# Optimization experiments

Hardware: AMD Instinct MI355X
Metric: run time of the kernel (lower is better)

The kernel has to match this reference:

```python
import jax, jax.numpy as jnp
import numpy as np

N_FULL, N_LOCAL, N_GLOBAL = 6, 4, 2
N_HEADS = N_FULL + N_LOCAL + N_GLOBAL
WINDOW = 64
DIM = 1536
B, S = 2, 2048


def setup_inputs() -> dict:
    key = jax.random.key(0)
    k0, k1, k2 = jax.random.split(key, 3)
    sc = DIM ** -0.5
    return {
        "x": jax.random.normal(k0, (B, S, DIM), dtype=jnp.float32),
        "Wqkv": jax.random.normal(k1, (DIM, 3 * DIM), dtype=jnp.float32) * sc,
        "bqkv": jnp.zeros((3 * DIM,), dtype=jnp.float32),
        "Wout": jax.random.normal(k2, (DIM, DIM), dtype=jnp.float32) * sc,
        "bout": jnp.zeros((DIM,), dtype=jnp.float32),
    }


def _attend(q, k, v, scale, bias=None):
    # q,k,v: [B,H,S,D]
    scores = jnp.einsum("bhqd,bhkd->bhqk", q, k) * scale
    if bias is not None:
        scores = scores + bias
    p = jax.nn.softmax(scores, axis=-1)
    return jnp.einsum("bhqk,bhkd->bhqd", p, v)


def reference(x, Wqkv, bqkv, Wout, bout):
    Bb, Ss, D = x.shape
    hd = D // N_HEADS
    scale = hd ** -0.5
    qkv = (x @ Wqkv + bqkv).reshape(Bb, Ss, 3, N_HEADS, hd)
    qkv = jnp.transpose(qkv, (2, 0, 3, 1, 4))  # [3,B,H,S,hd]
    q, k, v = qkv[0], qkv[1], qkv[2]
    h1 = N_FULL
    h2 = N_FULL + N_LOCAL

    # tier 1: full attention on first n_full heads
    out_full = _attend(q[:, :h1], k[:, :h1], v[:, :h1], scale)

    # tier 2: sliding-window (|i-j| <= window//2 allowed) on next n_local heads
    idx = jnp.arange(Ss)
    allowed = jnp.abs(idx[:, None] - idx[None, :]) <= WINDOW // 2  # [S,S]
    bias = jnp.where(allowed, 0.0, -jnp.inf).astype(x.dtype)[None, None]
    out_local = _attend(q[:, h1:h2], k[:, h1:h2], v[:, h1:h2], scale, bias)

    # tier 3: global — attend only to first and last tokens
    kg = jnp.stack([k[:, h2:, 0], k[:, h2:, -1]], axis=2)  # [B,Hg,2,hd]
    vg = jnp.stack([v[:, h2:, 0], v[:, h2:, -1]], axis=2)
    out_global = _attend(q[:, h2:], kg, vg, scale)

    out = jnp.concatenate([out_full, out_local, out_global], axis=1)  # [B,H,S,hd]
    out = jnp.transpose(out, (0, 2, 1, 3)).reshape(Bb, Ss, D)
    return out @ Wout + bout
```

## Files before the change

kernel.cpp:

```cpp
#include <hip/hip_runtime.h>
#include <hip/hip_bf16.h>

#define SEQ    2048
#define TOK    4096
#define DMODEL 1536
#define QKVROW 4608
#define HD     128
#define SCALE  0.08838834764831845f

#define NSPLIT 4
#define KRANGE (SEQ / NSPLIT)
#define NPAIR  12
#define ROWS_P (NPAIR * SEQ)
#define OPART_ELEMS ((size_t)ROWS_P * HD)

typedef __attribute__((ext_vector_type(8))) short short8;
typedef __attribute__((ext_vector_type(4))) short short4v;
typedef __attribute__((ext_vector_type(4))) float f32x4;

__device__ __forceinline__ float b2f(short s) {
    union { unsigned u; float f; } x;
    x.u = ((unsigned)(unsigned short)s) << 16;
    return x.f;
}
__device__ __forceinline__ short f2b(float f) {
    union { float f; unsigned u; } x; x.f = f;
    unsigned u = x.u;
    unsigned r = (u + 0x7fffu + ((u >> 16) & 1u)) >> 16;
    return (short)r;
}

__device__ __forceinline__ void gld_lds16(const short* g, short* l) {
    __builtin_amdgcn_global_load_lds(
        (__attribute__((address_space(1))) void*)(g),
        (__attribute__((address_space(3))) void*)(l), 16, 0, 0);
}

#define CVT_BLOCKS  6144
#define TQKV_BLOCKS 1728
#define TOUT_BLOCKS 576

__device__ __forceinline__ void transpose_tile(
    const float* __restrict__ W, short* __restrict__ WT,
    int K, int N, int k0, int n0, int t, short (*tile)[65])
{
    {
        int j  = t & 63;
        int i0 = (t >> 6) * 16;
        for (int ii = 0; ii < 16; ++ii)
            tile[i0 + ii][j] = f2b(W[(size_t)(k0 + i0 + ii) * N + n0 + j]);
    }
    __syncthreads();
    {
        int i  = t & 63;
        int j0 = (t >> 6) * 16;
        for (int jj = 0; jj < 16; ++jj)
            WT[(size_t)(n0 + j0 + jj) * K + k0 + i] = tile[i][j0 + jj];
    }
}

__global__ __launch_bounds__(256) void prepass_k(
    const float* __restrict__ x, const float* __restrict__ Wqkv,
    const float* __restrict__ Wout, short* __restrict__ xb,
    short* __restrict__ WqkvT, short* __restrict__ WoutT)
{
    __shared__ short tile[64][65];
    const int bid = blockIdx.x;
    const int t   = threadIdx.x;
    if (bid < CVT_BLOCKS) {
        int i = bid * 1024 + t * 4;
        float4 v = *(const float4*)(x + i);
        short4v b = { f2b(v.x), f2b(v.y), f2b(v.z), f2b(v.w) };
        *(short4v*)(xb + i) = b;
    } else if (bid < CVT_BLOCKS + TQKV_BLOCKS) {
        int tb = bid - CVT_BLOCKS;
        transpose_tile(Wqkv, WqkvT, DMODEL, QKVROW,
                       (tb / (QKVROW / 64)) * 64, (tb % (QKVROW / 64)) * 64, t, tile);
    } else {
        int tb = bid - (CVT_BLOCKS + TQKV_BLOCKS);
        transpose_tile(Wout, WoutT, DMODEL, DMODEL,
                       (tb / (DMODEL / 64)) * 64, (tb % (DMODEL / 64)) * 64, t, tile);
    }
}

template <bool OUT_BF16>
__global__ __launch_bounds__(256) void gemm_tn_k(
    const short* __restrict__ A, const short* __restrict__ BT,
    const float* __restrict__ bias, void* __restrict__ Cout,
    int M, int N, int K)
{
    __shared__ short As[128 * 32];
    __shared__ short Bs[128 * 32];

    const int t    = threadIdx.x;
    const int wave = t >> 6;
    const int lane = t & 63;
    const int quad = lane >> 4;
    const int lo   = lane & 15;
    const int m0   = blockIdx.y * 128;
    const int n0   = blockIdx.x * 128;
    const int wm   = (wave >> 1) * 64;
    const int wn   = (wave & 1) * 64;

    const int srow = wave * 16 + (lane >> 2);
    const int scol = (lane & 3) * 8;

    const short* aP0 = A  + (size_t)(m0 + srow) * K + scol;
    const short* aP1 = A  + (size_t)(m0 + 64 + srow) * K + scol;
    const short* bP0 = BT + (size_t)(n0 + srow) * K + scol;
    const short* bP1 = BT + (size_t)(n0 + 64 + srow) * K + scol;
    short* asD0 = As + (wave * 16) * 32;
    short* asD1 = As + (64 + wave * 16) * 32;
    short* bsD0 = Bs + (wave * 16) * 32;
    short* bsD1 = Bs + (64 + wave * 16) * 32;

    f32x4 acc[4][4];
    for (int i = 0; i < 4; ++i)
        for (int j = 0; j < 4; ++j)
            acc[i][j] = (f32x4){0.f, 0.f, 0.f, 0.f};

    for (int kt = 0; kt < K; kt += 32) {
        gld_lds16(aP0 + kt, asD0);
        gld_lds16(aP1 + kt, asD1);
        gld_lds16(bP0 + kt, bsD0);
        gld_lds16(bP1 + kt, bsD1);
        __syncthreads();

        short8 af[4], bfv[4];
        for (int i = 0; i < 4; ++i) {
            af[i]  = *(const short8*)(As + (wm + i * 16 + lo) * 32 + quad * 8);
            bfv[i] = *(const short8*)(Bs + (wn + i * 16 + lo) * 32 + quad * 8);
        }
        for (int mi = 0; mi < 4; ++mi)
            for (int ni = 0; ni < 4; ++ni)
                acc[mi][ni] = __builtin_amdgcn_mfma_f32_16x16x32_bf16(
                    af[mi], bfv[ni], acc[mi][ni], 0, 0, 0);
        __syncthreads();
    }

    for (int ni = 0; ni < 4; ++ni) {
        int col  = n0 + wn + ni * 16 + lo;
        float bv = bias[col];
        for (int mi = 0; mi < 4; ++mi)
            for (int r = 0; r < 4; ++r) {
                int row = m0 + wm + mi * 16 + quad * 4 + r;
                float val = acc[mi][ni][r] + bv;
                if (OUT_BF16)
                    ((short*)Cout)[(size_t)row * N + col] = f2b(val);
                else
                    ((float*)Cout)[(size_t)row * N + col] = val;
            }
    }
}

#define KSP 136
#define VTP 44
#define PLP 40

__global__ __launch_bounds__(256) void attn_full_split(
    const short* __restrict__ qkv, short* __restrict__ Opart,
    float* __restrict__ lsum)
{
    const int pair = blockIdx.y;
    const int b    = pair / 6;
    const int h    = pair % 6;
    const int q0   = blockIdx.x * 64;
    const int kz   = blockIdx.z;
    const int t    = threadIdx.x;
    const int wave = t >> 6;
    const int lane = t & 63;
    const int quad = lane >> 4;
    const int lo   = lane & 15;

    __shared__ short Ks[32 * KSP];
    __shared__ short Vr[32 * KSP];
    __shared__ short Vt[128 * VTP];
    __shared__ short Pl[4][16 * PLP];

    const short* base = qkv + (size_t)b * SEQ * QKVROW;

    short8 qf[4];
    {
        int qrow = q0 + wave * 16 + lo;
        const short* qp = base + (size_t)qrow * QKVROW + h * HD;
        for (int c = 0; c < 4; ++c)
            qf[c] = *(const short8*)(qp + c * 32 + quad * 8);
    }

    f32x4 o[8];
    for (int i = 0; i < 8; ++i) o[i] = (f32x4){0.f, 0.f, 0.f, 0.f};
    float lrow[4] = {0.f, 0.f, 0.f, 0.f};

    const int skey = t >> 3;
    const int sdc  = (t & 7) * 16;
    const int thd  = t & 127;
    const int tkc  = (t >> 7) * 16;

    const int kend = kz * KRANGE + KRANGE;
    for (int k0 = kz * KRANGE; k0 < kend; k0 += 32) {
        {
            const short* kro = base + (size_t)(k0 + skey) * QKVROW + DMODEL     + h * HD + sdc;
            const short* vro = base + (size_t)(k0 + skey) * QKVROW + 2 * DMODEL + h * HD + sdc;
            short8 ka = *(const short8*)kro;
            short8 kb = *(const short8*)(kro + 8);
            short8 va = *(const short8*)vro;
            short8 vb = *(const short8*)(vro + 8);
            *(short8*)(Ks + skey * KSP + sdc)     = ka;
            *(short8*)(Ks + skey * KSP + sdc + 8) = kb;
            *(short8*)(Vr + skey * KSP + sdc)     = va;
            *(short8*)(Vr + skey * KSP + sdc + 8) = vb;
        }
        __syncthreads();

        {
            short8 x0, x1;
            for (int j = 0; j < 8; ++j) x0[j] = Vr[(tkc + j) * KSP + thd];
            for (int j = 0; j < 8; ++j) x1[j] = Vr[(tkc + 8 + j) * KSP + thd];
            *(short8*)(Vt + thd * VTP + tkc)     = x0;
            *(short8*)(Vt + thd * VTP + tkc + 8) = x1;
        }

        f32x4 s[2];
        s[0] = (f32x4){0.f, 0.f, 0.f, 0.f};
        s[1] = (f32x4){0.f, 0.f, 0.f, 0.f};
        for (int g = 0; g < 2; ++g)
            for (int c = 0; c < 4; ++c) {
                short8 kf = *(const short8*)(Ks + (g * 16 + lo) * KSP + c * 32 + quad * 8);
                s[g] = __builtin_amdgcn_mfma_f32_16x16x32_bf16(qf[c], kf, s[g], 0, 0, 0);
            }

        for (int g = 0; g < 2; ++g)
            for (int r = 0; r < 4; ++r) {
                float p = __expf(s[g][r] * SCALE);
                lrow[r] += p;
                Pl[wave][(quad * 4 + r) * PLP + g * 16 + lo] = f2b(p);
            }
        __syncthreads();

        short8 pf = *(const short8*)(&Pl[wave][lo * PLP + quad * 8]);
        for (int ni = 0; ni < 8; ++ni) {
            short8 vf = *(const short8*)(Vt + (ni * 16 + lo) * VTP + quad * 8);
            o[ni] = __builtin_amdgcn_mfma_f32_16x16x32_bf16(pf, vf, o[ni], 0, 0, 0);
        }
    }

    for (int r = 0; r < 4; ++r)
        for (int off = 1; off < 16; off <<= 1)
            lrow[r] += __shfl_xor(lrow[r], off, 64);

    for (int ni = 0; ni < 8; ++ni)
        for (int r = 0; r < 4; ++r) {
            int grow = pair * SEQ + q0 + wave * 16 + quad * 4 + r;
            Opart[(size_t)kz * OPART_ELEMS + (size_t)grow * HD + ni * 16 + lo] =
                f2b(o[ni][r]);
        }
    if (lo == 0)
        for (int r = 0; r < 4; ++r) {
            int grow = pair * SEQ + q0 + wave * 16 + quad * 4 + r;
            lsum[kz * ROWS_P + grow] = lrow[r];
        }
}

__global__ __launch_bounds__(256) void attn_local_mfma(
    const short* __restrict__ qkv, short* __restrict__ att)
{
    const int pair = blockIdx.y;
    const int b    = pair >> 2;
    const int h    = 6 + (pair & 3);
    const int q0   = blockIdx.x * 64;
    const int t    = threadIdx.x;
    const int wave = t >> 6;
    const int lane = t & 63;
    const int quad = lane >> 4;
    const int lo   = lane & 15;

    __shared__ short Ks[32 * KSP];
    __shared__ short Vr[32 * KSP];
    __shared__ short Vt[128 * VTP];
    __shared__ short Pl[4][16 * PLP];

    const short* base = qkv + (size_t)b * SEQ * QKVROW;

    short8 qf[4];
    {
        int qrow = q0 + wave * 16 + lo;
        const short* qp = base + (size_t)qrow * QKVROW + h * HD;
        for (int c = 0; c < 4; ++c)
            qf[c] = *(const short8*)(qp + c * 32 + quad * 8);
    }

    f32x4 o[8];
    for (int i = 0; i < 8; ++i) o[i] = (f32x4){0.f, 0.f, 0.f, 0.f};
    float lrow[4] = {0.f, 0.f, 0.f, 0.f};

    const int skey = t >> 3;
    const int sdc  = (t & 7) * 16;
    const int thd  = t & 127;
    const int tkc  = (t >> 7) * 16;
    const int irow = q0 + wave * 16 + quad * 4;

    const int ks = max(0, q0 - 32);
    const int ke = min(SEQ, q0 + 96);
    for (int k0 = ks; k0 < ke; k0 += 32) {
        {
            const short* kro = base + (size_t)(k0 + skey) * QKVROW + DMODEL     + h * HD + sdc;
            const short* vro = base + (size_t)(k0 + skey) * QKVROW + 2 * DMODEL + h * HD + sdc;
            short8 ka = *(const short8*)kro;
            short8 kb = *(const short8*)(kro + 8);
            short8 va = *(const short8*)vro;
            short8 vb = *(const short8*)(vro + 8);
            *(short8*)(Ks + skey * KSP + sdc)     = ka;
            *(short8*)(Ks + skey * KSP + sdc + 8) = kb;
            *(short8*)(Vr + skey * KSP + sdc)     = va;
            *(short8*)(Vr + skey * KSP + sdc + 8) = vb;
        }
        __syncthreads();

        {
            short8 x0, x1;
            for (int j = 0; j < 8; ++j) x0[j] = Vr[(tkc + j) * KSP + thd];
            for (int j = 0; j < 8; ++j) x1[j] = Vr[(tkc + 8 + j) * KSP + thd];
            *(short8*)(Vt + thd * VTP + tkc)     = x0;
            *(short8*)(Vt + thd * VTP + tkc + 8) = x1;
        }

        f32x4 s[2];
        s[0] = (f32x4){0.f, 0.f, 0.f, 0.f};
        s[1] = (f32x4){0.f, 0.f, 0.f, 0.f};
        for (int g = 0; g < 2; ++g)
            for (int c = 0; c < 4; ++c) {
                short8 kf = *(const short8*)(Ks + (g * 16 + lo) * KSP + c * 32 + quad * 8);
                s[g] = __builtin_amdgcn_mfma_f32_16x16x32_bf16(qf[c], kf, s[g], 0, 0, 0);
            }

        for (int g = 0; g < 2; ++g)
            for (int r = 0; r < 4; ++r) {
                int j = k0 + g * 16 + lo;
                int d = irow + r - j;
                float p = (d >= -32 && d <= 32) ? __expf(s[g][r] * SCALE) : 0.f;
                lrow[r] += p;
                Pl[wave][(quad * 4 + r) * PLP + g * 16 + lo] = f2b(p);
            }
        __syncthreads();

        short8 pf = *(const short8*)(&Pl[wave][lo * PLP + quad * 8]);
        for (int ni = 0; ni < 8; ++ni) {
            short8 vf = *(const short8*)(Vt + (ni * 16 + lo) * VTP + quad * 8);
            o[ni] = __builtin_amdgcn_mfma_f32_16x16x32_bf16(pf, vf, o[ni], 0, 0, 0);
        }
    }

    for (int r = 0; r < 4; ++r)
        for (int off = 1; off < 16; off <<= 1)
            lrow[r] += __shfl_xor(lrow[r], off, 64);

    for (int ni = 0; ni < 8; ++ni)
        for (int r = 0; r < 4; ++r) {
            int row = irow + r;
            size_t off = ((size_t)(b * SEQ + row)) * DMODEL + h * HD + ni * 16 + lo;
            att[off] = f2b(o[ni][r] / lrow[r]);
        }
}

#define MERGE_BLOCKS  12288
#define GLOBAL_BLOCKS 2048

__global__ __launch_bounds__(256) void postattn_k(
    const short* __restrict__ qkv, const short* __restrict__ Opart,
    const float* __restrict__ lsum, short* __restrict__ att)
{
    const int bid  = blockIdx.x;
    const int t    = threadIdx.x;
    const int wave = t >> 6;
    const int lane = t & 63;

    if (bid < MERGE_BLOCKS) {
        int idx  = bid * 256 + t;
        int pair = idx >> 18;
        int q    = (idx >> 7) & (SEQ - 1);
        int hd   = idx & (HD - 1);
        int row  = pair * SEQ + q;
        float osum = 0.f, ls = 0.f;
        for (int z = 0; z < NSPLIT; ++z) {
            ls   += lsum[z * ROWS_P + row];
            osum += b2f(Opart[(size_t)z * OPART_ELEMS + (size_t)row * HD + hd]);
        }
        int b = pair / 6, h = pair % 6;
        att[((size_t)(b * SEQ + q)) * DMODEL + h * HD + hd] = f2b(osum / ls);
    } else {
        int gb   = bid - MERGE_BLOCKS;
        int pair = gb >> 9;
        int q    = (gb & 511) * 4 + wave;
        int b    = pair >> 1;
        int h    = 10 + (pair & 1);

        const short* base = qkv + (size_t)b * SEQ * QKVROW;
        const short* qp   = base + (size_t)q * QKVROW + h * HD;
        const short* k0   = base + DMODEL + h * HD;
        const short* k1   = base + (size_t)(SEQ - 1) * QKVROW + DMODEL + h * HD;

        float s0 = fmaf(b2f(qp[lane]), b2f(k0[lane]),
                   b2f(qp[lane + 64]) * b2f(k0[lane + 64]));
        float s1 = fmaf(b2f(qp[lane]), b2f(k1[lane]),
                   b2f(qp[lane + 64]) * b2f(k1[lane + 64]));
        for (int off = 1; off < 64; off <<= 1) {
            s0 += __shfl_xor(s0, off, 64);
            s1 += __shfl_xor(s1, off, 64);
        }
        s0 *= SCALE; s1 *= SCALE;
        float m  = fmaxf(s0, s1);
        float e0 = __expf(s0 - m), e1 = __expf(s1 - m);
        float inv = 1.f / (e0 + e1);
        float p0 = e0 * inv, p1 = e1 * inv;

        const short* v0 = base + 2 * DMODEL + h * HD;
        const short* v1 = base + (size_t)(SEQ - 1) * QKVROW + 2 * DMODEL + h * HD;
        size_t ob = ((size_t)(b * SEQ + q)) * DMODEL + h * HD;
        att[ob + lane]      = f2b(fmaf(p0, b2f(v0[lane]),      p1 * b2f(v1[lane])));
        att[ob + lane + 64] = f2b(fmaf(p0, b2f(v0[lane + 64]), p1 * b2f(v1[lane + 64])));
    }
}

extern "C" void kernel_launch(void* const* d_in, const int* in_sizes, int n_in,
                              void* d_out, int out_size, void* d_ws, size_t ws_size,
                              hipStream_t stream) {
    const float* x    = (const float*)d_in[0];
    const float* Wqkv = (const float*)d_in[1];
    const float* bqkv = (const float*)d_in[2];
    const float* Wout = (const float*)d_in[3];
    const float* bout = (const float*)d_in[4];

    char* p = (char*)d_ws;
    short* qkv   = (short*)p;  p += (size_t)TOK * QKVROW * 2;
    short* Opart = (short*)p;  p += OPART_ELEMS * NSPLIT * 2;
    float* lsum  = (float*)p;  p += (size_t)ROWS_P * NSPLIT * 4;
    short* xb    = (short*)p;  p += (size_t)TOK * DMODEL * 2;
    short* att   = xb;
    short* WqkvT = (short*)p;  p += (size_t)QKVROW * DMODEL * 2;
    short* WoutT = (short*)p;

    prepass_k<<<dim3(CVT_BLOCKS + TQKV_BLOCKS + TOUT_BLOCKS), 256, 0, stream>>>(
        x, Wqkv, Wout, xb, WqkvT, WoutT);
    gemm_tn_k<true><<<dim3(QKVROW / 128, TOK / 128), 256, 0, stream>>>(
        xb, WqkvT, bqkv, (void*)qkv, TOK, QKVROW, DMODEL);
    attn_full_split<<<dim3(SEQ / 64, NPAIR, NSPLIT), 256, 0, stream>>>(qkv, Opart, lsum);
    attn_local_mfma<<<dim3(SEQ / 64, 8), 256, 0, stream>>>(qkv, att);
    postattn_k<<<dim3(MERGE_BLOCKS + GLOBAL_BLOCKS), 256, 0, stream>>>(
        qkv, Opart, lsum, att);
    gemm_tn_k<false><<<dim3(DMODEL / 128, TOK / 128), 256, 0, stream>>>(
        att, WoutT, bout, d_out, TOK, DMODEL, DMODEL);
}
```

Measured before the change: 312.8 us.

## Replace GEMM with 256x256-tile 8-wave kernel using double-buffered 8-phase LDS pipeline

Result: slower. 345.8 us (+10.5%).

```diff
diff --git a/kernel.cpp b/kernel.cpp
--- a/kernel.cpp
+++ b/kernel.cpp
@@ -83,68 +83,129 @@
     }
 }
 
+__device__ __forceinline__ short* ldsP(short* base, int slot, int mat, int kh, int st) {
+    return base + (((slot * 2 + mat) * 2 + kh) * 16 + st) * 512;
+}
+
+template <int SLOT, int KH, int G>
+__device__ __forceinline__ void ld_a(short8 af[4], short* smem, int wm8, int lane) {
+#pragma unroll
+    for (int mi = 0; mi < 4; ++mi)
+        af[mi] = *(const short8*)(ldsP(smem, SLOT, 0, KH, wm8 + G * 4 + mi) + lane * 8);
+}
+template <int SLOT, int KH>
+__device__ __forceinline__ void ld_b(short8 bf[4], short* smem, int wn4, int lane) {
+#pragma unroll
+    for (int ni = 0; ni < 4; ++ni)
+        bf[ni] = *(const short8*)(ldsP(smem, SLOT, 1, KH, wn4 + ni) + lane * 8);
+}
+template <int G>
+__device__ __forceinline__ void mfma16(f32x4 (&acc)[8][4], const short8 af[4], const short8 bf[4]) {
+#pragma unroll
+    for (int mi = 0; mi < 4; ++mi)
+#pragma unroll
+        for (int ni = 0; ni < 4; ++ni)
+            acc[G * 4 + mi][ni] = __builtin_amdgcn_mfma_f32_16x16x32_bf16(
+                af[mi], bf[ni], acc[G * 4 + mi][ni], 0, 0, 0);
+}
+
+__device__ __forceinline__ void stage2(const short* g0, const short* g1, int ko,
+                                       short* d0, short* d1) {
+    gld_lds16(g0 + ko, d0);
+    gld_lds16(g1 + ko, d1);
+}
+
+#define STG_A(S, KH, KT) stage2(gA0, gA1, (KT) * 64 + (KH) * 32, \
+        ldsP(smem, (S), 0, (KH), wave), ldsP(smem, (S), 0, (KH), 8 + wave))
+#define STG_B(S, KH, KT) stage2(gB0, gB1, (KT) * 64 + (KH) * 32, \
+        ldsP(smem, (S), 1, (KH), wave), ldsP(smem, (S), 1, (KH), 8 + wave))
+
+#define PH(S, KH, G, LOADB, STG_STMT, VMW)                          \
+    do {                                                            \
+        ld_a<S, KH, G>(af, smem, wm8, lane);                        \
+        if (LOADB) ld_b<S, KH>(bf, smem, wn4, lane);                \
+        STG_STMT;                                                   \
+        asm volatile("" ::: "memory");                              \
+        __builtin_amdgcn_s_barrier();                               \
+        asm volatile("s_waitcnt lgkmcnt(0)" ::: "memory");          \
+        __builtin_amdgcn_s_setprio(1);                              \
+        mfma16<G>(acc, af, bf);                                     \
+        __builtin_amdgcn_s_setprio(0);                              \
+        if (VMW) asm volatile("s_waitcnt vmcnt(6)" ::: "memory");   \
+        asm volatile("" ::: "memory");                              \
+        __builtin_amdgcn_s_barrier();                               \
+        asm volatile("" ::: "memory");                              \
+    } while (0)
+
 template <bool OUT_BF16>
-__global__ __launch_bounds__(256) void gemm_tn_k(
+__global__ __launch_bounds__(512, 2) void gemm256_8ph(
     const short* __restrict__ A, const short* __restrict__ BT,
     const float* __restrict__ bias, void* __restrict__ Cout,
-    int M, int N, int K)
+    int N, int K)
 {
-    __shared__ short As[128 * 32];
-    __shared__ short Bs[128 * 32];
+    __shared__ short smem[2 * 2 * 2 * 16 * 512];
 
     const int t    = threadIdx.x;
     const int wave = t >> 6;
     const int lane = t & 63;
     const int quad = lane >> 4;
     const int lo   = lane & 15;
-    const int m0   = blockIdx.y * 128;
-    const int n0   = blockIdx.x * 128;
-    const int wm   = (wave >> 1) * 64;
-    const int wn   = (wave & 1) * 64;
-
-    const int srow = wave * 16 + (lane >> 2);
-    const int scol = (lane & 3) * 8;
-
-    const short* aP0 = A  + (size_t)(m0 + srow) * K + scol;
-    const short* aP1 = A  + (size_t)(m0 + 64 + srow) * K + scol;
-    const short* bP0 = BT + (size_t)(n0 + srow) * K + scol;
-    const short* bP1 = BT + (size_t)(n0 + 64 + srow) * K + scol;
-    short* asD0 = As + (wave * 16) * 32;
-    short* asD1 = As + (64 + wave * 16) * 32;
-    short* bsD0 = Bs + (wave * 16) * 32;
-    short* bsD1 = Bs + (64 + wave * 16) * 32;
-
-    f32x4 acc[4][4];
-    for (int i = 0; i < 4; ++i)
+    const int wm   = wave >> 2;
+    const int wn   = wave & 3;
+    const int wm8  = wm * 8;
+    const int wn4  = wn * 4;
+    const int bn0  = blockIdx.x * 256;
+    const int bm0  = blockIdx.y * 256;
+
+    const int rO = quad * 8;
+    const short* gA0 = A  + (size_t)(bm0 + wave * 16 + lo) * K + rO;
+    const short* gA1 = A  + (size_t)(bm0 + (8 + wave) * 16 + lo) * K + rO;
+    const short* gB0 = BT + (size_t)(bn0 + wave * 16 + lo) * K + rO;
+    const short* gB1 = BT + (size_t)(bn0 + (8 + wave) * 16 + lo) * K + rO;
+
+    f32x4 acc[8][4];
+#pragma unroll
+    for (int i = 0; i < 8; ++i)
+#pragma unroll
         for (int j = 0; j < 4; ++j)
             acc[i][j] = (f32x4){0.f, 0.f, 0.f, 0.f};
 
-    for (int kt = 0; kt < K; kt += 32) {
-        gld_lds16(aP0 + kt, asD0);
-        gld_lds16(aP1 + kt, asD1);
-        gld_lds16(bP0 + kt, bsD0);
-        gld_lds16(bP1 + kt, bsD1);
-        __syncthreads();
-
-        short8 af[4], bfv[4];
-        for (int i = 0; i < 4; ++i) {
-            af[i]  = *(const short8*)(As + (wm + i * 16 + lo) * 32 + quad * 8);
-            bfv[i] = *(const short8*)(Bs + (wn + i * 16 + lo) * 32 + quad * 8);
-        }
-        for (int mi = 0; mi < 4; ++mi)
-            for (int ni = 0; ni < 4; ++ni)
-                acc[mi][ni] = __builtin_amdgcn_mfma_f32_16x16x32_bf16(
-                    af[mi], bfv[ni], acc[mi][ni], 0, 0, 0);
-        __syncthreads();
-    }
-
+    const int NT = K >> 6;
+
+    STG_A(0, 0, 0); STG_A(0, 1, 0); STG_B(0, 0, 0); STG_B(0, 1, 0);
+    STG_B(1, 0, 1); STG_A(1, 0, 1); STG_B(1, 1, 1);
+    asm volatile("s_waitcnt vmcnt(6)" ::: "memory");
+    asm volatile("" ::: "memory");
+    __builtin_amdgcn_s_barrier();
+    asm volatile("" ::: "memory");
+
+    short8 af[4], bf[4];
+#pragma unroll 1
+    for (int it = 0; it < (NT >> 1); ++it) {
+        const int T  = it * 2;
+        const int t2 = min(T + 2, NT - 1);
+        const int t3 = min(T + 3, NT - 1);
+        PH(0, 0, 0, true,  STG_A(1, 1, T + 1), 0);
+        PH(0, 0, 1, false, STG_B(0, 0, t2),    0);
+        PH(0, 1, 0, true,  STG_A(0, 0, t2),    0);
+        PH(0, 1, 1, false, STG_B(0, 1, t2),    1);
+        PH(1, 0, 0, true,  STG_A(0, 1, t2),    0);
+        PH(1, 0, 1, false, STG_B(1, 0, t3),    0);
+        PH(1, 1, 0, true,  STG_A(1, 0, t3),    0);
+        PH(1, 1, 1, false, STG_B(1, 1, t3),    1);
+    }
+    asm volatile("s_waitcnt vmcnt(0)" ::: "memory");
+
+#pragma unroll
     for (int ni = 0; ni < 4; ++ni) {
-        int col  = n0 + wn + ni * 16 + lo;
+        int col  = bn0 + wn * 64 + ni * 16 + lo;
         float bv = bias[col];
-        for (int mi = 0; mi < 4; ++mi)
+#pragma unroll
+        for (int r8 = 0; r8 < 8; ++r8)
+#pragma unroll
             for (int r = 0; r < 4; ++r) {
-                int row = m0 + wm + mi * 16 + quad * 4 + r;
-                float val = acc[mi][ni][r] + bv;
+                int row   = bm0 + wm * 128 + r8 * 16 + quad * 4 + r;
+                float val = acc[r8][ni][r] + bv;
                 if (OUT_BF16)
                     ((short*)Cout)[(size_t)row * N + col] = f2b(val);
                 else
@@ -441,12 +502,12 @@
 
     prepass_k<<<dim3(CVT_BLOCKS + TQKV_BLOCKS + TOUT_BLOCKS), 256, 0, stream>>>(
         x, Wqkv, Wout, xb, WqkvT, WoutT);
-    gemm_tn_k<true><<<dim3(QKVROW / 128, TOK / 128), 256, 0, stream>>>(
-        xb, WqkvT, bqkv, (void*)qkv, TOK, QKVROW, DMODEL);
+    gemm256_8ph<true><<<dim3(QKVROW / 256, TOK / 256), 512, 0, stream>>>(
+        xb, WqkvT, bqkv, (void*)qkv, QKVROW, DMODEL);
     attn_full_split<<<dim3(SEQ / 64, NPAIR, NSPLIT), 256, 0, stream>>>(qkv, Opart, lsum);
     attn_local_mfma<<<dim3(SEQ / 64, 8), 256, 0, stream>>>(qkv, att);
     postattn_k<<<dim3(MERGE_BLOCKS + GLOBAL_BLOCKS), 256, 0, stream>>>(
         qkv, Opart, lsum, att);
-    gemm_tn_k<false><<<dim3(DMODEL / 128, TOK / 128), 256, 0, stream>>>(
-        att, WoutT, bout, d_out, TOK, DMODEL, DMODEL);
-}
+    gemm256_8ph<false><<<dim3(DMODEL / 256, TOK / 256), 512, 0, stream>>>(
+        att, WoutT, bout, d_out, DMODEL, DMODEL);
+}
```

## Pre-transpose V globally and double-buffer K/V tiles in full attention

Applied to the files above, without the earlier changes.

New measurement: 294.1 us. -6.0%, faster.

```diff
diff --git a/kernel.cpp b/kernel.cpp
--- a/kernel.cpp
+++ b/kernel.cpp
@@ -153,112 +153,153 @@
     }
 }
 
+#define VT_BLOCKS 768
+
+__global__ __launch_bounds__(256) void vtrans_k(
+    const short* __restrict__ qkv, short* __restrict__ vT)
+{
+    __shared__ short tile[64][65];
+    const int bid = blockIdx.x;
+    const int t   = threadIdx.x;
+    const int bh  = bid >> 6;
+    const int rem = bid & 63;
+    const int st  = rem & 31, dt = rem >> 5;
+    const int b   = bh / 6, h = bh % 6;
+    const int s0  = st * 64, d0 = dt * 64;
+
+    const short* src = qkv + (size_t)(b * SEQ + s0) * QKVROW + 2 * DMODEL + h * HD + d0;
+    {
+        int j = t & 63, i0 = (t >> 6) * 16;
+        for (int ii = 0; ii < 16; ++ii)
+            tile[i0 + ii][j] = src[(size_t)(i0 + ii) * QKVROW + j];
+    }
+    __syncthreads();
+    {
+        int i = t & 63, j0 = (t >> 6) * 16;
+        short* dst = vT + ((size_t)(b * 6 + h) * HD + d0) * SEQ + s0;
+        for (int jj = 0; jj < 16; ++jj)
+            dst[(size_t)(j0 + jj) * SEQ + i] = tile[i][j0 + jj];
+    }
+}
+
 #define KSP 136
 #define VTP 44
 #define PLP 40
 
-__global__ __launch_bounds__(256) void attn_full_split(
-    const short* __restrict__ qkv, short* __restrict__ Opart,
-    float* __restrict__ lsum)
+__global__ __launch_bounds__(256, 3) void attn_full_v2(
+    const short* __restrict__ qkv, const short* __restrict__ vT,
+    short* __restrict__ Opart, float* __restrict__ lsum)
 {
     const int pair = blockIdx.y;
     const int b    = pair / 6;
     const int h    = pair % 6;
-    const int q0   = blockIdx.x * 64;
+    const int q0   = blockIdx.x * 128;
     const int kz   = blockIdx.z;
     const int t    = threadIdx.x;
-    const int wave = t >> 6;
+    const int w    = t >> 6;
     const int lane = t & 63;
     const int quad = lane >> 4;
     const int lo   = lane & 15;
 
-    __shared__ short Ks[32 * KSP];
-    __shared__ short Vr[32 * KSP];
-    __shared__ short Vt[128 * VTP];
-    __shared__ short Pl[4][16 * PLP];
+    __shared__ short KV[2][2][8][512];
+    __shared__ short Pl[4][2][16 * PLP];
 
     const short* base = qkv + (size_t)b * SEQ * QKVROW;
 
-    short8 qf[4];
-    {
-        int qrow = q0 + wave * 16 + lo;
-        const short* qp = base + (size_t)qrow * QKVROW + h * HD;
+    short8 qf[2][4];
+#pragma unroll
+    for (int u = 0; u < 2; ++u) {
+        const short* qp = base + (size_t)(q0 + w * 32 + u * 16 + lo) * QKVROW + h * HD;
+#pragma unroll
         for (int c = 0; c < 4; ++c)
-            qf[c] = *(const short8*)(qp + c * 32 + quad * 8);
-    }
-
-    f32x4 o[8];
-    for (int i = 0; i < 8; ++i) o[i] = (f32x4){0.f, 0.f, 0.f, 0.f};
-    float lrow[4] = {0.f, 0.f, 0.f, 0.f};
-
-    const int skey = t >> 3;
-    const int sdc  = (t & 7) * 16;
-    const int thd  = t & 127;
-    const int tkc  = (t >> 7) * 16;
-
-    const int kend = kz * KRANGE + KRANGE;
-    for (int k0 = kz * KRANGE; k0 < kend; k0 += 32) {
-        {
-            const short* kro = base + (size_t)(k0 + skey) * QKVROW + DMODEL     + h * HD + sdc;
-            const short* vro = base + (size_t)(k0 + skey) * QKVROW + 2 * DMODEL + h * HD + sdc;
-            short8 ka = *(const short8*)kro;
-            short8 kb = *(const short8*)(kro + 8);
-            short8 va = *(const short8*)vro;
-            short8 vb = *(const short8*)(vro + 8);
-            *(short8*)(Ks + skey * KSP + sdc)     = ka;
-            *(short8*)(Ks + skey * KSP + sdc + 8) = kb;
-            *(short8*)(Vr + skey * KSP + sdc)     = va;
-            *(short8*)(Vr + skey * KSP + sdc + 8) = vb;
+            qf[u][c] = *(const short8*)(qp + c * 32 + quad * 8);
+    }
+
+    f32x4 o[2][8];
+#pragma unroll
+    for (int u = 0; u < 2; ++u)
+#pragma unroll
+        for (int i = 0; i < 8; ++i)
+            o[u][i] = (f32x4){0.f, 0.f, 0.f, 0.f};
+    float lrow[2][4] = {{0.f, 0.f, 0.f, 0.f}, {0.f, 0.f, 0.f, 0.f}};
+
+    const int k0s = kz * KRANGE;
+    const short* kp0 = base + (size_t)(k0s + lo) * QKVROW      + DMODEL + h * HD + w * 32 + quad * 8;
+    const short* kp1 = base + (size_t)(k0s + 16 + lo) * QKVROW + DMODEL + h * HD + w * 32 + quad * 8;
+    const short* vbase = vT + ((size_t)(b * 6 + h) * HD) * SEQ;
+    const short* vp0 = vbase + (size_t)(w * 16 + lo) * SEQ       + k0s + quad * 8;
+    const short* vp1 = vbase + (size_t)((w + 4) * 16 + lo) * SEQ + k0s + quad * 8;
+
+#define AFS_STG(SL, KT)                                                     \
+    do {                                                                    \
+        gld_lds16(kp0 + (size_t)(KT) * 32 * QKVROW, &KV[SL][0][w][0]);      \
+        gld_lds16(kp1 + (size_t)(KT) * 32 * QKVROW, &KV[SL][0][w + 4][0]);  \
+        gld_lds16(vp0 + (KT) * 32, &KV[SL][1][w][0]);                       \
+        gld_lds16(vp1 + (KT) * 32, &KV[SL][1][w + 4][0]);                   \
+    } while (0)
+
+    AFS_STG(0, 0);
+    __syncthreads();
+
+    const int NT_ = KRANGE / 32;
+#pragma unroll 1
+    for (int kt = 0; kt < NT_; ++kt) {
+        const int sl = kt & 1;
+        if (kt + 1 < NT_) AFS_STG(sl ^ 1, kt + 1);
+
+        f32x4 s[2][2];
+        s[0][0] = s[0][1] = s[1][0] = s[1][1] = (f32x4){0.f, 0.f, 0.f, 0.f};
+#pragma unroll
+        for (int g = 0; g < 2; ++g)
+#pragma unroll
+            for (int c = 0; c < 4; ++c) {
+                short8 kf = *(const short8*)(&KV[sl][0][g * 4 + c][lane * 8]);
+                s[0][g] = __builtin_amdgcn_mfma_f32_16x16x32_bf16(qf[0][c], kf, s[0][g], 0, 0, 0);
+                s[1][g] = __builtin_amdgcn_mfma_f32_16x16x32_bf16(qf[1][c], kf, s[1][g], 0, 0, 0);
+            }
+
+#pragma unroll
+        for (int u = 0; u < 2; ++u)
+#pragma unroll
+            for (int g = 0; g < 2; ++g)
+#pragma unroll
+                for (int r = 0; r < 4; ++r) {
+                    float p = __expf(s[u][g][r] * SCALE);
+                    lrow[u][r] += p;
+                    Pl[w][u][(quad * 4 + r) * PLP + g * 16 + lo] = f2b(p);
+                }
+        short8 pf0 = *(const short8*)(&Pl[w][0][lo * PLP + quad * 8]);
+        short8 pf1 = *(const short8*)(&Pl[w][1][lo * PLP + quad * 8]);
+
+#pragma unroll
+        for (int ni = 0; ni < 8; ++ni) {
+            short8 vf = *(const short8*)(&KV[sl][1][ni][lane * 8]);
+            o[0][ni] = __builtin_amdgcn_mfma_f32_16x16x32_bf16(pf0, vf, o[0][ni], 0, 0, 0);
+            o[1][ni] = __builtin_amdgcn_mfma_f32_16x16x32_bf16(pf1, vf, o[1][ni], 0, 0, 0);
         }
         __syncthreads();
-
-        {
-            short8 x0, x1;
-            for (int j = 0; j < 8; ++j) x0[j] = Vr[(tkc + j) * KSP + thd];
-            for (int j = 0; j < 8; ++j) x1[j] = Vr[(tkc + 8 + j) * KSP + thd];
-            *(short8*)(Vt + thd * VTP + tkc)     = x0;
-            *(short8*)(Vt + thd * VTP + tkc + 8) = x1;
-        }
-
-        f32x4 s[2];
-        s[0] = (f32x4){0.f, 0.f, 0.f, 0.f};
-        s[1] = (f32x4){0.f, 0.f, 0.f, 0.f};
-        for (int g = 0; g < 2; ++g)
-            for (int c = 0; c < 4; ++c) {
-                short8 kf = *(const short8*)(Ks + (g * 16 + lo) * KSP + c * 32 + quad * 8);
-                s[g] = __builtin_amdgcn_mfma_f32_16x16x32_bf16(qf[c], kf, s[g], 0, 0, 0);
-            }
-
-        for (int g = 0; g < 2; ++g)
+    }
+#undef AFS_STG
+
+    for (int u = 0; u < 2; ++u)
+        for (int r = 0; r < 4; ++r)
+            for (int off = 1; off < 16; off <<= 1)
+                lrow[u][r] += __shfl_xor(lrow[u][r], off, 64);
+
+#pragma unroll
+    for (int u = 0; u < 2; ++u)
+        for (int ni = 0; ni < 8; ++ni)
             for (int r = 0; r < 4; ++r) {
-                float p = __expf(s[g][r] * SCALE);
-                lrow[r] += p;
-                Pl[wave][(quad * 4 + r) * PLP + g * 16 + lo] = f2b(p);
-            }
-        __syncthreads();
-
-        short8 pf = *(const short8*)(&Pl[wave][lo * PLP + quad * 8]);
-        for (int ni = 0; ni < 8; ++ni) {
-            short8 vf = *(const short8*)(Vt + (ni * 16 + lo) * VTP + quad * 8);
-            o[ni] = __builtin_amdgcn_mfma_f32_16x16x32_bf16(pf, vf, o[ni], 0, 0, 0);
-        }
-    }
-
-    for (int r = 0; r < 4; ++r)
-        for (int off = 1; off < 16; off <<= 1)
-            lrow[r] += __shfl_xor(lrow[r], off, 64);
-
-    for (int ni = 0; ni < 8; ++ni)
-        for (int r = 0; r < 4; ++r) {
-            int grow = pair * SEQ + q0 + wave * 16 + quad * 4 + r;
-            Opart[(size_t)kz * OPART_ELEMS + (size_t)grow * HD + ni * 16 + lo] =
-                f2b(o[ni][r]);
-        }
+                int grow = pair * SEQ + q0 + w * 32 + u * 16 + quad * 4 + r;
+                Opart[(size_t)kz * OPART_ELEMS + (size_t)grow * HD + ni * 16 + lo] =
+                    f2b(o[u][ni][r]);
+            }
     if (lo == 0)
-        for (int r = 0; r < 4; ++r) {
-            int grow = pair * SEQ + q0 + wave * 16 + quad * 4 + r;
-            lsum[kz * ROWS_P + grow] = lrow[r];
-        }
+        for (int u = 0; u < 2; ++u)
+            for (int r = 0; r < 4; ++r) {
+                int grow = pair * SEQ + q0 + w * 32 + u * 16 + quad * 4 + r;
+                lsum[kz * ROWS_P + grow] = lrow[u][r];
+            }
 }
 
 __global__ __launch_bounds__(256) void attn_local_mfma(
@@ -437,13 +478,16 @@
     short* xb    = (short*)p;  p += (size_t)TOK * DMODEL * 2;
     short* att   = xb;
     short* WqkvT = (short*)p;  p += (size_t)QKVROW * DMODEL * 2;
+    short* vT    = WqkvT;
     short* WoutT = (short*)p;
 
     prepass_k<<<dim3(CVT_BLOCKS + TQKV_BLOCKS + TOUT_BLOCKS), 256, 0, stream>>>(
         x, Wqkv, Wout, xb, WqkvT, WoutT);
     gemm_tn_k<true><<<dim3(QKVROW / 128, TOK / 128), 256, 0, stream>>>(
         xb, WqkvT, bqkv, (void*)qkv, TOK, QKVROW, DMODEL);
-    attn_full_split<<<dim3(SEQ / 64, NPAIR, NSPLIT), 256, 0, stream>>>(qkv, Opart, lsum);
+    vtrans_k<<<dim3(VT_BLOCKS), 256, 0, stream>>>(qkv, vT);
+    attn_full_v2<<<dim3(SEQ / 128, NPAIR, NSPLIT), 256, 0, stream>>>(
+        qkv, vT, Opart, lsum);
     attn_local_mfma<<<dim3(SEQ / 64, 8), 256, 0, stream>>>(qkv, att);
     postattn_k<<<dim3(MERGE_BLOCKS + GLOBAL_BLOCKS), 256, 0, stream>>>(
         qkv, Opart, lsum, att);
```
